# Kernel tuning notes

Hardware: AMD Instinct MI355X
Metric: run time of the kernel (lower is better)

The kernel has to match this reference:

```python
import jax, jax.numpy as jnp
import numpy as np

D = 384      # pct_dim == spm_dim == d_model
H = 6        # heads
DK = D // H  # 64
HID = 96     # int(384 * 0.25)
B = 8
NS = 2040    # multiple of 85 (SPM pyramid 64+16+4+1 groups)
NP = 2048


def _ln(x, g, b, eps):
    m = x.mean(-1, keepdims=True)
    v = jnp.mean((x - m) ** 2, -1, keepdims=True)
    return (x - m) * jax.lax.rsqrt(v + eps) * g + b


def setup_inputs() -> dict:
    key = jax.random.key(0)
    ks = jax.random.split(key, 10)
    w = lambda k, shape: jax.random.normal(k, shape, jnp.float32) * 0.02
    p = {
        "spm_feature": jax.random.normal(ks[0], (B, NS, D), jnp.float32),
        "pct_feature": jax.random.normal(ks[1], (B, NP, D), jnp.float32),
        # extractor pre-norms (eps=1e-6)
        "pct_g": jnp.ones(D), "pct_b": jnp.zeros(D),
        "spm_g": jnp.ones(D), "spm_b": jnp.zeros(D),
        # CrossAttention internal norms (eps=1e-5)
        "lnx_g": jnp.ones(D), "lnx_b": jnp.zeros(D),
        "lny_g": jnp.ones(D), "lny_b": jnp.zeros(D),
        "Wq": w(ks[2], (D, D)), "bq": jnp.zeros(D),
        "Wk": w(ks[3], (D, D)), "bk": jnp.zeros(D),
        "Wv": w(ks[4], (D, D)), "bv": jnp.zeros(D),
        # 1x1 Conv1d in CrossAttention
        "Wc": w(ks[5], (D, D)), "bc": jnp.zeros(D),
        "lnc_g": jnp.ones(D), "lnc_b": jnp.zeros(D),
        # FFN
        "ffn_g": jnp.ones(D), "ffn_b": jnp.zeros(D),
        "W1": w(ks[6], (HID, D)), "b1": jnp.zeros(HID),
        "Wdw": w(ks[7], (HID, HID)), "bdw": jnp.zeros(HID),
        "W2": w(ks[8], (D, HID)), "b2": jnp.zeros(D),
    }
    return p


def reference(spm_feature, pct_feature, pct_g, pct_b, spm_g, spm_b,
              lnx_g, lnx_b, lny_g, lny_b, Wq, bq, Wk, bk, Wv, bv,
              Wc, bc, lnc_g, lnc_b, ffn_g, ffn_b, W1, b1, Wdw, bdw, W2, b2):
    EPS6, EPS5 = 1e-6, 1e-5
    # extractor pre-norms (the (N,B,C) permutes in the torch code cancel for LN)
    x = _ln(spm_feature, spm_g, spm_b, EPS6)
    y = _ln(pct_feature, pct_g, pct_b, EPS6)
    # CrossAttention's own (double) LayerNorms
    xn = _ln(x, lnx_g, lnx_b, EPS5)
    yn = _ln(y, lny_g, lny_b, EPS5)
    Bq, Nq, _ = xn.shape
    q = (xn @ Wq.T + bq).reshape(Bq, Nq, H, DK)
    k = (yn @ Wk.T + bk).reshape(Bq, -1, H, DK)
    v = (yn @ Wv.T + bv).reshape(Bq, -1, H, DK)
    scale = 1.0 / np.sqrt(DK).astype(np.float32)
    scores = jnp.einsum('bqhd,bkhd->bhqk', q, k) * scale
    att = jax.nn.softmax(scores, axis=-1)
    # non-standard extra renormalization across the HEAD dimension (dim=1)
    att = att / (1e-9 + att.sum(axis=1, keepdims=True))
    o = jnp.einsum('bhqk,bkhd->bqhd', att, v).reshape(Bq, Nq, D)
    qf = q.reshape(Bq, Nq, D)
    r = (qf - o) @ Wc.T + bc            # 1x1 Conv1d == channel linear
    r = _ln(r, lnc_g, lnc_b, EPS5)
    r = jnp.where(r > 0, r, 0.02 * r)    # LeakyReLU(0.02)
    cross = qf + r
    spm = spm_feature + cross            # first residual
    # FFN: fc1 -> (4-way segment split, shared 1x1 dwconv1, concat) -> gelu -> fc2
    # a 1x1 Conv1d with shared weights applied to contiguous segments then
    # concatenated is mathematically identical to one application on the full seq
    h = _ln(spm, ffn_g, ffn_b, EPS5)
    h = h @ W1.T + b1                    # (B, NS, 96)
    h = h @ Wdw.T + bdw                  # shared 1x1 conv over channels
    h = jax.nn.gelu(h, approximate=False)
    h = h @ W2.T + b2                    # (B, NS, 384)
    return spm + h
```

## Files before the change

kernel.cpp:

```cpp
#include <hip/hip_runtime.h>
#include <hip/hip_bf16.h>
#include <math.h>

#define D 384
#define NHEAD 6
#define DKH 64
#define HID 96
#define BB 8
#define NS 2040
#define NPK 2048

typedef __attribute__((ext_vector_type(8))) short short8;
typedef __attribute__((ext_vector_type(4))) short short4v;
typedef __attribute__((ext_vector_type(4))) float f32x4;

__device__ __forceinline__ float bf2f(ushort u) {
  union { uint u; float f; } x; x.u = ((uint)u) << 16; return x.f;
}
__device__ __forceinline__ ushort f2bf(float f) {
  union { float f; uint u; } x; x.f = f;
  uint r = x.u + 0x7fffu + ((x.u >> 16) & 1u);
  return (ushort)(r >> 16);
}
__device__ __forceinline__ float ldin(const void* p, size_t i, bool f32) {
  return f32 ? ((const float*)p)[i] : bf2f(((const ushort*)p)[i]);
}
__device__ __forceinline__ uint4 load8bf(const void* p, size_t off, bool f32) {
  if (!f32) return *(const uint4*)((const ushort*)p + off);
  const float* f = (const float*)p + off;
  float4 a = *(const float4*)f, b = *(const float4*)(f + 4);
  uint4 r;
  r.x = (uint)f2bf(a.x) | ((uint)f2bf(a.y) << 16);
  r.y = (uint)f2bf(a.z) | ((uint)f2bf(a.w) << 16);
  r.z = (uint)f2bf(b.x) | ((uint)f2bf(b.y) << 16);
  r.w = (uint)f2bf(b.z) | ((uint)f2bf(b.w) << 16);
  return r;
}
__device__ __forceinline__ uint bfsub3(uint a, uint p0, uint p1) {
  float lo = bf2f((ushort)(a & 0xffffu)) - (bf2f((ushort)(p0 & 0xffffu)) + bf2f((ushort)(p1 & 0xffffu)));
  float hi = bf2f((ushort)(a >> 16))     - (bf2f((ushort)(p0 >> 16))     + bf2f((ushort)(p1 >> 16)));
  return (uint)f2bf(lo) | ((uint)f2bf(hi) << 16);
}

__global__ void probe_dtype(const void* ones_vec, int* flg) {
  if (threadIdx.x == 0 && blockIdx.x == 0) {
    uint u = *(const uint*)ones_vec;
    *flg = (u == 0x3F800000u) ? 1 : 0;
  }
}

__global__ __launch_bounds__(256) void ln2_kernel(
    const void* __restrict__ src,
    const void* __restrict__ g1, const void* __restrict__ b1,
    const void* __restrict__ g2, const void* __restrict__ b2,
    ushort* __restrict__ dst, const int* __restrict__ flg,
    int rows, float eps1, float eps2)
{
  const bool f32 = *flg != 0;
  int row = blockIdx.x * 4 + (threadIdx.x >> 6);
  int lane = threadIdx.x & 63;
  if (row >= rows) return;
  float v[6];
#pragma unroll
  for (int j = 0; j < 3; ++j) {
    int c = 2 * (lane + 64 * j);
    v[2*j]   = ldin(src, (size_t)row * D + c,     f32);
    v[2*j+1] = ldin(src, (size_t)row * D + c + 1, f32);
  }
  float s = 0.f, s2 = 0.f;
#pragma unroll
  for (int i = 0; i < 6; ++i) { s += v[i]; s2 += v[i]*v[i]; }
#pragma unroll
  for (int off = 32; off; off >>= 1) { s += __shfl_xor(s, off); s2 += __shfl_xor(s2, off); }
  float mean = s * (1.f/D);
  float rstd = rsqrtf(fmaxf(s2*(1.f/D) - mean*mean, 0.f) + eps1);
  float t[6];
  float u = 0.f, u2 = 0.f;
#pragma unroll
  for (int j = 0; j < 3; ++j) {
    int c = 2 * (lane + 64 * j);
#pragma unroll
    for (int i = 0; i < 2; ++i) {
      float val = (v[2*j+i] - mean) * rstd * ldin(g1, c+i, f32) + ldin(b1, c+i, f32);
      t[2*j+i] = val; u += val; u2 += val*val;
    }
  }
#pragma unroll
  for (int off = 32; off; off >>= 1) { u += __shfl_xor(u, off); u2 += __shfl_xor(u2, off); }
  float mean2 = u * (1.f/D);
  float rstd2 = rsqrtf(fmaxf(u2*(1.f/D) - mean2*mean2, 0.f) + eps2);
  ushort* q = dst + (size_t)row * D;
#pragma unroll
  for (int j = 0; j < 3; ++j) {
    int c = 2 * (lane + 64 * j);
    ushort lo = f2bf((t[2*j]   - mean2) * rstd2 * ldin(g2, c,   f32) + ldin(b2, c,   f32));
    ushort hi = f2bf((t[2*j+1] - mean2) * rstd2 * ldin(g2, c+1, f32) + ldin(b2, c+1, f32));
    *(uint*)(q + c) = (uint)lo | ((uint)hi << 16);
  }
}

template<int EPI, int ASUB>
__global__ __launch_bounds__(256) void gemm_bt(
    const ushort* __restrict__ A, const ushort* __restrict__ A2,
    const ushort* __restrict__ A3,
    const void* __restrict__ W, const void* __restrict__ bias,
    const ushort* __restrict__ resid, void* __restrict__ Cout,
    const int* __restrict__ flg, int M, int N, int K)
{
  const bool f32 = *flg != 0;
  __shared__ ushort As[64][40];
  __shared__ ushort Ws[64][40];
  int tm = blockIdx.x * 64, tn = blockIdx.y * 64;
  int tid = threadIdx.x;
  int wv = tid >> 6, lane = tid & 63;
  f32x4 acc[4] = {{0,0,0,0},{0,0,0,0},{0,0,0,0},{0,0,0,0}};
  int lrow = tid >> 2, lc8 = (tid & 3) * 8;
  for (int k0 = 0; k0 < K; k0 += 32) {
    __syncthreads();
    uint4 aval = *(const uint4*)(A + (size_t)(tm + lrow) * K + k0 + lc8);
    if (ASUB) {
      uint4 bval = *(const uint4*)(A2 + (size_t)(tm + lrow) * K + k0 + lc8);
      uint4 cval = *(const uint4*)(A3 + (size_t)(tm + lrow) * K + k0 + lc8);
      aval.x = bfsub3(aval.x, bval.x, cval.x); aval.y = bfsub3(aval.y, bval.y, cval.y);
      aval.z = bfsub3(aval.z, bval.z, cval.z); aval.w = bfsub3(aval.w, bval.w, cval.w);
    }
    *(uint4*)&As[lrow][lc8] = aval;
    uint4 wval = make_uint4(0,0,0,0);
    int wr = tn + lrow;
    if (wr < N) wval = load8bf(W, (size_t)wr * K + k0 + lc8, f32);
    *(uint4*)&Ws[lrow][lc8] = wval;
    __syncthreads();
    short8 af = *(const short8*)&As[16*wv + (lane & 15)][8*(lane >> 4)];
#pragma unroll
    for (int n = 0; n < 4; ++n) {
      short8 bfr = *(const short8*)&Ws[16*n + (lane & 15)][8*(lane >> 4)];
      acc[n] = __builtin_amdgcn_mfma_f32_16x16x32_bf16(af, bfr, acc[n], 0, 0, 0);
    }
  }
  int rbase = tm + 16*wv + 4*(lane >> 4);
#pragma unroll
  for (int n = 0; n < 4; ++n) {
    int col = tn + 16*n + (lane & 15);
    if (col >= N) continue;
    float bv = ldin(bias, col, f32);
#pragma unroll
    for (int e = 0; e < 4; ++e) {
      int row = rbase + e;
      float val = acc[n][e] + bv;
      if (EPI == 1) val = 0.5f * val * (1.f + erff(val * 0.70710678118654752f));
      if (EPI == 2) val += bf2f(resid[(size_t)row * N + col]);
      if (EPI == 2 && f32) {
        ((float*)Cout)[(size_t)row * N + col] = val;
      } else {
        ((ushort*)Cout)[(size_t)row * N + col] = f2bf(val);
      }
    }
  }
}

__global__ __launch_bounds__(256) void vt_tr(
    const ushort* __restrict__ v, ushort* __restrict__ vt)
{
  __shared__ ushort T[64][66];
  int k0 = blockIdx.x * 64, d0 = blockIdx.y * 64, b = blockIdx.z;
  int tid = threadIdx.x;
#pragma unroll
  for (int i = 0; i < 2; ++i) {
    int f = tid + 256*i;
    int r = f >> 3, c8 = (f & 7) * 8;
    uint4 w = *(const uint4*)(v + (size_t)(b*NPK + k0 + r)*D + d0 + c8);
    const ushort* wsp = (const ushort*)&w;
#pragma unroll
    for (int j = 0; j < 8; ++j) T[r][c8 + j] = wsp[j];
  }
  __syncthreads();
#pragma unroll
  for (int i = 0; i < 2; ++i) {
    int f = tid + 256*i;
    int r = f >> 3, c8 = (f & 7) * 8;
    ushort tmp[8];
#pragma unroll
    for (int j = 0; j < 8; ++j) tmp[j] = T[c8 + j][r];
    *(uint4*)(vt + (size_t)(b*D + d0 + r)*NPK + k0 + c8) = *(const uint4*)tmp;
  }
}

__global__ __launch_bounds__(256) void attn_mz(
    const ushort* __restrict__ q, const ushort* __restrict__ k,
    float* __restrict__ mmout)
{
  __shared__ ushort Ksh[64][72];
  int qt = blockIdx.x, h = blockIdx.y, b = blockIdx.z;
  int tid = threadIdx.x, wv = tid >> 6, lane = tid & 63;
  int l15 = lane & 15, l4 = lane >> 4;
  int q0 = qt*64 + wv*16;
  const float C = 0.18033688011112042f;
  int qrow = q0 + l15; if (qrow > NS-1) qrow = NS-1;
  const ushort* qp = q + (size_t)(b*NS + qrow)*D + h*64 + l4*8;
  short8 qf0 = *(const short8*)(qp);
  short8 qf1 = *(const short8*)(qp + 32);
  float m[4] = {-1e30f,-1e30f,-1e30f,-1e30f};
  float z[4] = {0.f,0.f,0.f,0.f};
  for (int kt = 0; kt < NPK; kt += 64) {
    __syncthreads();
#pragma unroll
    for (int i = 0; i < 2; ++i) {
      int f = tid + 256*i;
      int r = f >> 3, c8 = (f & 7) * 8;
      *(uint4*)&Ksh[r][c8] = *(const uint4*)(k + (size_t)(b*NPK + kt + r)*D + h*64 + c8);
    }
    __syncthreads();
#pragma unroll
    for (int ks = 0; ks < 4; ++ks) {
      short8 b0 = *(const short8*)&Ksh[ks*16 + l15][l4*8];
      short8 b1 = *(const short8*)&Ksh[ks*16 + l15][32 + l4*8];
      f32x4 t = {0.f,0.f,0.f,0.f};
      t = __builtin_amdgcn_mfma_f32_16x16x32_bf16(qf0, b0, t, 0, 0, 0);
      t = __builtin_amdgcn_mfma_f32_16x16x32_bf16(qf1, b1, t, 0, 0, 0);
#pragma unroll
      for (int e = 0; e < 4; ++e) {
        float u = t[e] * C;
        float mn = fmaxf(m[e], u);
        z[e] = z[e]*exp2f(m[e]-mn) + exp2f(u-mn);
        m[e] = mn;
      }
    }
  }
#pragma unroll
  for (int off = 1; off < 16; off <<= 1) {
#pragma unroll
    for (int e = 0; e < 4; ++e) {
      float mo = __shfl_xor(m[e], off);
      float zo = __shfl_xor(z[e], off);
      float mn = fmaxf(m[e], mo);
      z[e] = z[e]*exp2f(m[e]-mn) + zo*exp2f(mo-mn);
      m[e] = mn;
    }
  }
  if (l15 == 0) {
#pragma unroll
    for (int e = 0; e < 4; ++e) {
      int row = q0 + l4*4 + e;
      if (row < NS) mmout[(size_t)(b*NHEAD + h)*NS + row] = m[e] + log2f(z[e]);
    }
  }
}

__global__ __launch_bounds__(256, 2) void attn_pv(
    const ushort* __restrict__ q, const ushort* __restrict__ k,
    const ushort* __restrict__ vt, const float* __restrict__ mm,
    ushort* __restrict__ op0, ushort* __restrict__ op1)
{
  __shared__ ushort Ks[32][392];
  __shared__ ushort Vt[384][40];
  int wgid = blockIdx.x;
  int b = wgid & 7, qt = (wgid >> 3) & 31, sl = wgid >> 8;
  ushort* opart = sl ? op1 : op0;
  int tid = threadIdx.x, wv = tid >> 6, lane = tid & 63;
  int l15 = lane & 15, l4 = lane >> 4;
  int q0 = qt*64 + wv*16;
  const float C = 0.18033688011112042f;
  int qrow = q0 + l15; if (qrow > NS-1) qrow = NS-1;
  short8 qf[12];
#pragma unroll
  for (int c = 0; c < 12; ++c)
    qf[c] = *(const short8*)(q + (size_t)(b*NS + qrow)*D + c*32 + l4*8);
  float mmr[6];
#pragma unroll
  for (int h = 0; h < 6; ++h)
    mmr[h] = mm[(size_t)(b*NHEAD + h)*NS + qrow];
  f32x4 acc[6][4];
#pragma unroll
  for (int h = 0; h < 6; ++h)
#pragma unroll
    for (int n = 0; n < 4; ++n) acc[h][n] = f32x4{0.f,0.f,0.f,0.f};

  for (int kt = sl*1024; kt < sl*1024 + 1024; kt += 32) {
    __syncthreads();
#pragma unroll
    for (int i = 0; i < 6; ++i) {
      int f = tid + 256*i;
      int r = f / 48, c = (f % 48) * 8;
      *(uint4*)&Ks[r][c] = *(const uint4*)(k + (size_t)(b*NPK + kt + r)*D + c);
    }
#pragma unroll
    for (int i = 0; i < 6; ++i) {
      int f = tid + 256*i;
      int r = f >> 2, c8 = (f & 3) * 8;
      *(uint4*)&Vt[r][c8] = *(const uint4*)(vt + (size_t)(b*D + r)*NPK + kt + c8);
    }
    __syncthreads();
    f32x4 s[6][2];
    __builtin_amdgcn_s_setprio(1);
#pragma unroll
    for (int h = 0; h < 6; ++h)
#pragma unroll
      for (int ks = 0; ks < 2; ++ks) {
        short8 a0 = *(const short8*)&Ks[ks*16 + l15][h*64 + l4*8];
        short8 a1 = *(const short8*)&Ks[ks*16 + l15][h*64 + 32 + l4*8];
        f32x4 t = {0.f,0.f,0.f,0.f};
        t = __builtin_amdgcn_mfma_f32_16x16x32_bf16(a0, qf[2*h],   t, 0, 0, 0);
        t = __builtin_amdgcn_mfma_f32_16x16x32_bf16(a1, qf[2*h+1], t, 0, 0, 0);
        s[h][ks] = t;
      }
    __builtin_amdgcn_s_setprio(0);
    short4v pa[6][2];
#pragma unroll
    for (int ks = 0; ks < 2; ++ks) {
#pragma unroll
      for (int e = 0; e < 4; ++e) {
        float w6[6];
        float sum = 1e-9f;
#pragma unroll
        for (int h = 0; h < 6; ++h) {
          w6[h] = exp2f(s[h][ks][e]*C - mmr[h]);
          sum += w6[h];
        }
        float inv = __builtin_amdgcn_rcpf(sum);
#pragma unroll
        for (int h = 0; h < 6; ++h) s[h][ks][e] = w6[h]*inv;
      }
#pragma unroll
      for (int h = 0; h < 6; ++h) {
        short4v p;
        p[0] = (short)f2bf(s[h][ks][0]);
        p[1] = (short)f2bf(s[h][ks][1]);
        p[2] = (short)f2bf(s[h][ks][2]);
        p[3] = (short)f2bf(s[h][ks][3]);
        pa[h][ks] = p;
      }
    }
    __builtin_amdgcn_s_setprio(1);
#pragma unroll
    for (int h = 0; h < 6; ++h)
#pragma unroll
      for (int n = 0; n < 4; ++n)
#pragma unroll
        for (int ks = 0; ks < 2; ++ks) {
          short4v vb4 = *(const short4v*)&Vt[h*64 + 16*n + l15][ks*16 + l4*4];
          acc[h][n] = __builtin_amdgcn_mfma_f32_16x16x16bf16_1k(pa[h][ks], vb4, acc[h][n], 0, 0, 0);
        }
    __builtin_amdgcn_s_setprio(0);
  }
#pragma unroll
  for (int h = 0; h < 6; ++h)
#pragma unroll
    for (int n = 0; n < 4; ++n)
#pragma unroll
      for (int e = 0; e < 4; ++e) {
        int row = q0 + l4*4 + e;
        if (row < NS) opart[(size_t)(b*NS + row)*D + h*64 + 16*n + l15] = f2bf(acc[h][n][e]);
      }
}

__global__ __launch_bounds__(256) void cross_ln(
    const ushort* __restrict__ rtmp, const ushort* __restrict__ q,
    const void* __restrict__ spm,
    const void* __restrict__ lg, const void* __restrict__ lb,
    const void* __restrict__ fg, const void* __restrict__ fb,
    ushort* __restrict__ spm2, ushort* __restrict__ hin,
    const int* __restrict__ flg, int rows)
{
  const bool f32 = *flg != 0;
  int row = blockIdx.x * 4 + (threadIdx.x >> 6);
  int lane = threadIdx.x & 63;
  if (row >= rows) return;
  const ushort* rp = rtmp + (size_t)row * D;
  float v[6];
#pragma unroll
  for (int j = 0; j < 3; ++j) {
    uint w = *(const uint*)(rp + 2*(lane + 64*j));
    v[2*j]   = bf2f((ushort)(w & 0xffffu));
    v[2*j+1] = bf2f((ushort)(w >> 16));
  }
  float s = 0.f, s2 = 0.f;
#pragma unroll
  for (int i = 0; i < 6; ++i) { s += v[i]; s2 += v[i]*v[i]; }
#pragma unroll
  for (int off = 32; off; off >>= 1) { s += __shfl_xor(s, off); s2 += __shfl_xor(s2, off); }
  float mean = s * (1.f/D);
  float rstd = rsqrtf(fmaxf(s2*(1.f/D) - mean*mean, 0.f) + 1e-5f);
  const ushort* qp = q + (size_t)row * D;
  ushort* op = spm2 + (size_t)row * D;
  float t[6];
  float u = 0.f, u2 = 0.f;
#pragma unroll
  for (int j = 0; j < 3; ++j) {
    int c = 2*(lane + 64*j);
#pragma unroll
    for (int i = 0; i < 2; ++i) {
      float r = (v[2*j+i] - mean)*rstd*ldin(lg, c+i, f32) + ldin(lb, c+i, f32);
      r = r > 0.f ? r : 0.02f*r;
      float ov = ldin(spm, (size_t)row*D + c + i, f32) + bf2f(qp[c+i]) + r;
      op[c+i] = f2bf(ov);
      t[2*j+i] = ov; u += ov; u2 += ov*ov;
    }
  }
#pragma unroll
  for (int off = 32; off; off >>= 1) { u += __shfl_xor(u, off); u2 += __shfl_xor(u2, off); }
  float mean2 = u * (1.f/D);
  float rstd2 = rsqrtf(fmaxf(u2*(1.f/D) - mean2*mean2, 0.f) + 1e-5f);
  ushort* hp = hin + (size_t)row * D;
#pragma unroll
  for (int j = 0; j < 3; ++j) {
    int c = 2*(lane + 64*j);
    ushort lo = f2bf((t[2*j]   - mean2)*rstd2*ldin(fg, c,   f32) + ldin(fb, c,   f32));
    ushort hi = f2bf((t[2*j+1] - mean2)*rstd2*ldin(fg, c+1, f32) + ldin(fb, c+1, f32));
    *(uint*)(hp + c) = (uint)lo | ((uint)hi << 16);
  }
}

extern "C" void kernel_launch(void* const* d_in, const int* in_sizes, int n_in,
                              void* d_out, int out_size, void* d_ws, size_t ws_size,
                              hipStream_t stream)
{
  const void* spm   = d_in[0];
  const void* pct   = d_in[1];
  const void* pct_g = d_in[2];
  const void* pct_b = d_in[3];
  const void* spm_g = d_in[4];
  const void* spm_b = d_in[5];
  const void* lnx_g = d_in[6];
  const void* lnx_b = d_in[7];
  const void* lny_g = d_in[8];
  const void* lny_b = d_in[9];
  const void* Wq = d_in[10]; const void* bq = d_in[11];
  const void* Wk = d_in[12]; const void* bk = d_in[13];
  const void* Wv = d_in[14]; const void* bv = d_in[15];
  const void* Wc = d_in[16]; const void* bc = d_in[17];
  const void* lnc_g = d_in[18]; const void* lnc_b = d_in[19];
  const void* ffn_g = d_in[20]; const void* ffn_b = d_in[21];
  const void* W1 = d_in[22];  const void* b1 = d_in[23];
  const void* Wdw = d_in[24]; const void* bdw = d_in[25];
  const void* W2 = d_in[26];  const void* b2 = d_in[27];

  char* ws = (char*)d_ws;
  int*    flg  = (int*)(ws + 0);
  ushort* kb   = (ushort*)(ws + 256);
  ushort* vb   = (ushort*)(ws + 12583168);
  ushort* qb   = (ushort*)(ws + 25166080);
  ushort* vtg  = (ushort*)(ws + 37699840);
  char*   R    = ws + 50282752;
  ushort* xn   = (ushort*)R;
  ushort* yn   = (ushort*)R;
  ushort* op1  = (ushort*)R;
  float*  mmb  = (float*)(R + 12533760);
  ushort* op0  = vb;
  ushort* rtmp = vtg;
  ushort* spm2 = kb;
  ushort* hin  = qb;
  ushort* h1   = (ushort*)R;
  ushort* h2   = (ushort*)(R + 3133440);

  const int M_S = BB * NS;
  const int M_P = BB * NPK;

  probe_dtype<<<1, 64, 0, stream>>>(pct_g, flg);
  ln2_kernel<<<M_S/4, 256, 0, stream>>>(spm, spm_g, spm_b, lnx_g, lnx_b, xn, flg, M_S, 1e-6f, 1e-5f);
  gemm_bt<0,0><<<dim3(M_S/64, 6), 256, 0, stream>>>(xn, nullptr, nullptr, Wq, bq, nullptr, qb, flg, M_S, D, D);
  ln2_kernel<<<M_P/4, 256, 0, stream>>>(pct, pct_g, pct_b, lny_g, lny_b, yn, flg, M_P, 1e-6f, 1e-5f);
  gemm_bt<0,0><<<dim3(M_P/64, 6), 256, 0, stream>>>(yn, nullptr, nullptr, Wk, bk, nullptr, kb, flg, M_P, D, D);
  gemm_bt<0,0><<<dim3(M_P/64, 6), 256, 0, stream>>>(yn, nullptr, nullptr, Wv, bv, nullptr, vb, flg, M_P, D, D);
  vt_tr<<<dim3(NPK/64, D/64, BB), 256, 0, stream>>>(vb, vtg);
  attn_mz<<<dim3(32, NHEAD, BB), 256, 0, stream>>>(qb, kb, mmb);
  attn_pv<<<512, 256, 0, stream>>>(qb, kb, vtg, mmb, op0, op1);
  gemm_bt<0,1><<<dim3(M_S/64, 6), 256, 0, stream>>>(qb, op0, op1, Wc, bc, nullptr, rtmp, flg, M_S, D, D);
  cross_ln<<<M_S/4, 256, 0, stream>>>(rtmp, qb, spm, lnc_g, lnc_b, ffn_g, ffn_b, spm2, hin, flg, M_S);
  gemm_bt<0,0><<<dim3(M_S/64, 2), 256, 0, stream>>>(hin, nullptr, nullptr, W1, b1, nullptr, h1, flg, M_S, HID, D);
  gemm_bt<1,0><<<dim3(M_S/64, 2), 256, 0, stream>>>(h1, nullptr, nullptr, Wdw, bdw, nullptr, h2, flg, M_S, HID, HID);
  gemm_bt<2,0><<<dim3(M_S/64, 6), 256, 0, stream>>>(h2, nullptr, nullptr, W2, b2, spm2, d_out, flg, M_S, D, HID);
}
```

Before: 555.4 us.

## Add 128x128-tile GEMM for D-wide projections and truncate P to bf16

Introduces a gemm128 kernel in which each 4-wave block computes a 128x128 output tile (each wave 64x64, a 4x4 grid of MFMAs) and clamps rows at the M boundary. It replaces the 64x64 gemm_bt for the Q/K/V, conv and fc2 projections, so operands are reused more per LDS load and fewer blocks are launched. Separately, the softmax probabilities are packed to bf16 by bit truncation instead of round-to-nearest-even, which cuts ALU work in the attention inner loop but adds a slight downward bias. Larger tiles also raise register pressure and give 384 blocks per GEMM, which may leave parts of the GPU idle.

Result: slower. 581.0 us (+4.6%).

```diff
diff --git a/kernel.cpp b/kernel.cpp
--- a/kernel.cpp
+++ b/kernel.cpp
@@ -99,12 +99,11 @@
   }
 }
 
-template<int EPI, int ASUB>
+template<int EPI>
 __global__ __launch_bounds__(256) void gemm_bt(
-    const ushort* __restrict__ A, const ushort* __restrict__ A2,
-    const ushort* __restrict__ A3,
+    const ushort* __restrict__ A,
     const void* __restrict__ W, const void* __restrict__ bias,
-    const ushort* __restrict__ resid, void* __restrict__ Cout,
+    void* __restrict__ Cout,
     const int* __restrict__ flg, int M, int N, int K)
 {
   const bool f32 = *flg != 0;
@@ -118,12 +117,6 @@
   for (int k0 = 0; k0 < K; k0 += 32) {
     __syncthreads();
     uint4 aval = *(const uint4*)(A + (size_t)(tm + lrow) * K + k0 + lc8);
-    if (ASUB) {
-      uint4 bval = *(const uint4*)(A2 + (size_t)(tm + lrow) * K + k0 + lc8);
-      uint4 cval = *(const uint4*)(A3 + (size_t)(tm + lrow) * K + k0 + lc8);
-      aval.x = bfsub3(aval.x, bval.x, cval.x); aval.y = bfsub3(aval.y, bval.y, cval.y);
-      aval.z = bfsub3(aval.z, bval.z, cval.z); aval.w = bfsub3(aval.w, bval.w, cval.w);
-    }
     *(uint4*)&As[lrow][lc8] = aval;
     uint4 wval = make_uint4(0,0,0,0);
     int wr = tn + lrow;
@@ -148,11 +141,79 @@
       int row = rbase + e;
       float val = acc[n][e] + bv;
       if (EPI == 1) val = 0.5f * val * (1.f + erff(val * 0.70710678118654752f));
-      if (EPI == 2) val += bf2f(resid[(size_t)row * N + col]);
-      if (EPI == 2 && f32) {
-        ((float*)Cout)[(size_t)row * N + col] = val;
-      } else {
-        ((ushort*)Cout)[(size_t)row * N + col] = f2bf(val);
+      ((ushort*)Cout)[(size_t)row * N + col] = f2bf(val);
+    }
+  }
+}
+
+template<int EPI, int ASUB>
+__global__ __launch_bounds__(256) void gemm128(
+    const ushort* __restrict__ A, const ushort* __restrict__ A2,
+    const ushort* __restrict__ A3,
+    const void* __restrict__ W, const void* __restrict__ bias,
+    const ushort* __restrict__ resid, void* __restrict__ Cout,
+    const int* __restrict__ flg, int M, int N, int K)
+{
+  const bool f32 = *flg != 0;
+  __shared__ ushort As[128][40];
+  __shared__ ushort Bs[128][40];
+  int tm = blockIdx.x * 128, tn = blockIdx.y * 128;
+  int tid = threadIdx.x;
+  int wv = tid >> 6, lane = tid & 63;
+  int l15 = lane & 15, l4 = lane >> 4;
+  int wr = wv >> 1, wc = wv & 1;
+  f32x4 acc[4][4];
+#pragma unroll
+  for (int m = 0; m < 4; ++m)
+#pragma unroll
+    for (int n = 0; n < 4; ++n) acc[m][n] = f32x4{0.f,0.f,0.f,0.f};
+  int lrow = tid >> 2, lc8 = (tid & 3) * 8;
+  for (int k0 = 0; k0 < K; k0 += 32) {
+    __syncthreads();
+#pragma unroll
+    for (int half = 0; half < 2; ++half) {
+      int ar = tm + lrow + 64*half;
+      if (ar > M-1) ar = M-1;
+      uint4 aval = *(const uint4*)(A + (size_t)ar * K + k0 + lc8);
+      if (ASUB) {
+        uint4 bval = *(const uint4*)(A2 + (size_t)ar * K + k0 + lc8);
+        uint4 cval = *(const uint4*)(A3 + (size_t)ar * K + k0 + lc8);
+        aval.x = bfsub3(aval.x, bval.x, cval.x); aval.y = bfsub3(aval.y, bval.y, cval.y);
+        aval.z = bfsub3(aval.z, bval.z, cval.z); aval.w = bfsub3(aval.w, bval.w, cval.w);
+      }
+      *(uint4*)&As[lrow + 64*half][lc8] = aval;
+      uint4 wvl = load8bf(W, (size_t)(tn + lrow + 64*half) * K + k0 + lc8, f32);
+      *(uint4*)&Bs[lrow + 64*half][lc8] = wvl;
+    }
+    __syncthreads();
+    short8 af[4], bfv[4];
+#pragma unroll
+    for (int m = 0; m < 4; ++m) af[m] = *(const short8*)&As[wr*64 + m*16 + l15][l4*8];
+#pragma unroll
+    for (int n = 0; n < 4; ++n) bfv[n] = *(const short8*)&Bs[wc*64 + n*16 + l15][l4*8];
+#pragma unroll
+    for (int m = 0; m < 4; ++m)
+#pragma unroll
+      for (int n = 0; n < 4; ++n)
+        acc[m][n] = __builtin_amdgcn_mfma_f32_16x16x32_bf16(af[m], bfv[n], acc[m][n], 0, 0, 0);
+  }
+#pragma unroll
+  for (int n = 0; n < 4; ++n) {
+    int col = tn + wc*64 + n*16 + l15;
+    float bv = ldin(bias, col, f32);
+#pragma unroll
+    for (int m = 0; m < 4; ++m) {
+#pragma unroll
+      for (int e = 0; e < 4; ++e) {
+        int row = tm + wr*64 + m*16 + 4*l4 + e;
+        if (row >= M) continue;
+        float val = acc[m][n][e] + bv;
+        if (EPI == 2) val += bf2f(resid[(size_t)row * N + col]);
+        if (EPI == 2 && f32) {
+          ((float*)Cout)[(size_t)row * N + col] = val;
+        } else {
+          ((ushort*)Cout)[(size_t)row * N + col] = f2bf(val);
+        }
       }
     }
   }
@@ -322,12 +383,14 @@
       }
 #pragma unroll
       for (int h = 0; h < 6; ++h) {
-        short4v p;
-        p[0] = (short)f2bf(s[h][ks][0]);
-        p[1] = (short)f2bf(s[h][ks][1]);
-        p[2] = (short)f2bf(s[h][ks][2]);
-        p[3] = (short)f2bf(s[h][ks][3]);
-        pa[h][ks] = p;
+        union { float f; uint u; } x0, x1, x2, x3;
+        x0.f = s[h][ks][0]; x1.f = s[h][ks][1];
+        x2.f = s[h][ks][2]; x3.f = s[h][ks][3];
+        uint lo = (x1.u & 0xFFFF0000u) | (x0.u >> 16);
+        uint hi = (x3.u & 0xFFFF0000u) | (x2.u >> 16);
+        union { uint2 u; short4v s4; } cv;
+        cv.u = make_uint2(lo, hi);
+        pa[h][ks] = cv.s4;
       }
     }
     __builtin_amdgcn_s_setprio(1);
@@ -457,16 +520,16 @@
 
   probe_dtype<<<1, 64, 0, stream>>>(pct_g, flg);
   ln2_kernel<<<M_S/4, 256, 0, stream>>>(spm, spm_g, spm_b, lnx_g, lnx_b, xn, flg, M_S, 1e-6f, 1e-5f);
-  gemm_bt<0,0><<<dim3(M_S/64, 6), 256, 0, stream>>>(xn, nullptr, nullptr, Wq, bq, nullptr, qb, flg, M_S, D, D);
+  gemm128<0,0><<<dim3(128, 3), 256, 0, stream>>>(xn, nullptr, nullptr, Wq, bq, nullptr, qb, flg, M_S, D, D);
   ln2_kernel<<<M_P/4, 256, 0, stream>>>(pct, pct_g, pct_b, lny_g, lny_b, yn, flg, M_P, 1e-6f, 1e-5f);
-  gemm_bt<0,0><<<dim3(M_P/64, 6), 256, 0, stream>>>(yn, nullptr, nullptr, Wk, bk, nullptr, kb, flg, M_P, D, D);
-  gemm_bt<0,0><<<dim3(M_P/64, 6), 256, 0, stream>>>(yn, nullptr, nullptr, Wv, bv, nullptr, vb, flg, M_P, D, D);
+  gemm128<0,0><<<dim3(128, 3), 256, 0, stream>>>(yn, nullptr, nullptr, Wk, bk, nullptr, kb, flg, M_P, D, D);
+  gemm128<0,0><<<dim3(128, 3), 256, 0, stream>>>(yn, nullptr, nullptr, Wv, bv, nullptr, vb, flg, M_P, D, D);
   vt_tr<<<dim3(NPK/64, D/64, BB), 256, 0, stream>>>(vb, vtg);
   attn_mz<<<dim3(32, NHEAD, BB), 256, 0, stream>>>(qb, kb, mmb);
   attn_pv<<<512, 256, 0, stream>>>(qb, kb, vtg, mmb, op0, op1);
-  gemm_bt<0,1><<<dim3(M_S/64, 6), 256, 0, stream>>>(qb, op0, op1, Wc, bc, nullptr, rtmp, flg, M_S, D, D);
+  gemm128<0,1><<<dim3(128, 3), 256, 0, stream>>>(qb, op0, op1, Wc, bc, nullptr, rtmp, flg, M_S, D, D);
   cross_ln<<<M_S/4, 256, 0, stream>>>(rtmp, qb, spm, lnc_g, lnc_b, ffn_g, ffn_b, spm2, hin, flg, M_S);
-  gemm_bt<0,0><<<dim3(M_S/64, 2), 256, 0, stream>>>(hin, nullptr, nullptr, W1, b1, nullptr, h1, flg, M_S, HID, D);
-  gemm_bt<1,0><<<dim3(M_S/64, 2), 256, 0, stream>>>(h1, nullptr, nullptr, Wdw, bdw, nullptr, h2, flg, M_S, HID, HID);
-  gemm_bt<2,0><<<dim3(M_S/64, 6), 256, 0, stream>>>(h2, nullptr, nullptr, W2, b2, spm2, d_out, flg, M_S, D, HID);
-}
+  gemm_bt<0><<<dim3(M_S/64, 2), 256, 0, stream>>>(hin, W1, b1, h1, flg, M_S, HID, D);
+  gemm_bt<1><<<dim3(M_S/64, 2), 256, 0, stream>>>(h1, Wdw, bdw, h2, flg, M_S, HID, HID);
+  gemm128<2,0><<<dim3(128, 3), 256, 0, stream>>>(h2, nullptr, nullptr, W2, b2, spm2, d_out, flg, M_S, D, HID);
+}
```
